# Performance work log

Measured on AMD Instinct MI355X. Metric: run time of the kernel, lower is better.

The kernel has to match this reference:

```python
import jax, jax.numpy as jnp
import numpy as np

NN_SIZE = 10  # k nearest neighbors (includes the point itself)
EPS = 1e-8


def batch_normals(points_nchw, nn_size):
    # points_nchw: (B, 3, N)
    x = jnp.transpose(points_nchw, (0, 2, 1))  # (B, N, 3)
    sq = jnp.sum(x * x, axis=-1)  # (B, N)
    # pairwise squared distances (B, N, N)
    d2 = sq[:, :, None] + sq[:, None, :] - 2.0 * jnp.einsum('bnd,bmd->bnm', x, x)
    _, idx = jax.lax.top_k(-d2, nn_size)  # (B, N, k) nearest-neighbor indices
    # irregular gather of neighborhoods: (B, N, k, 3)
    neigh = jax.vmap(lambda p, i: p[i])(x, idx)
    centered = neigh - jnp.mean(neigh, axis=2, keepdims=True)
    # local 3x3 covariance per point
    cov = jnp.einsum('bnki,bnkj->bnij', centered, centered) / nn_size
    _, vecs = jnp.linalg.eigh(cov)  # eigenvalues ascending
    normals = vecs[..., 0]  # eigenvector of smallest eigenvalue, (B, N, 3), unit norm
    return jnp.transpose(normals, (0, 2, 1))  # (B, 3, N)


def setup_inputs() -> dict:
    key = jax.random.key(0)
    k1, k2 = jax.random.split(key)
    pred = jax.random.normal(k1, (8, 3, 4096), dtype=jnp.float32)
    gt = jax.random.normal(k2, (8, 3, 4096), dtype=jnp.float32)
    return {"pred": pred, "gt": gt}


def reference(pred, gt):
    pn = batch_normals(pred, NN_SIZE)  # (B, 3, N)
    gn = batch_normals(gt, NN_SIZE)    # (B, 3, N)
    # cosine similarity along the channel (coordinate) dim
    dot = jnp.sum(pn * gn, axis=1)
    denom = jnp.sqrt(jnp.sum(pn * pn, axis=1)) * jnp.sqrt(jnp.sum(gn * gn, axis=1))
    cos = dot / jnp.maximum(denom, EPS)
    return jnp.mean(1.0 - jnp.abs(cos))
```

## Files before the change

### kernel.cpp

```cpp
#include <hip/hip_runtime.h>
#include <float.h>
#include <math.h>

#define BATCH 8
#define NPTS 4096
#define KNN 10
#define BN (BATCH * NPTS)

__device__ inline float med3f(float x, float a, float b) {
    return __builtin_amdgcn_fmed3f(x, a, b);
}

__device__ inline void smallest_eigvec(float a00, float a01, float a02,
                                       float a11, float a12, float a22,
                                       float& vx, float& vy, float& vz) {
    float p1 = a01 * a01 + a02 * a02 + a12 * a12;
    float q = (a00 + a11 + a22) * (1.0f / 3.0f);
    float b00 = a00 - q, b11 = a11 - q, b22 = a22 - q;
    float p2 = b00 * b00 + b11 * b11 + b22 * b22 + 2.0f * p1;
    float p = sqrtf(p2 * (1.0f / 6.0f));
    if (p < 1e-20f) { vx = 1.0f; vy = 0.0f; vz = 0.0f; return; }
    float ip = 1.0f / p;
    float c00 = b00 * ip, c01 = a01 * ip, c02 = a02 * ip;
    float c11 = b11 * ip, c12 = a12 * ip, c22 = b22 * ip;
    float detB = c00 * (c11 * c22 - c12 * c12)
               - c01 * (c01 * c22 - c12 * c02)
               + c02 * (c01 * c12 - c11 * c02);
    float r = 0.5f * detB;
    r = fminf(1.0f, fmaxf(-1.0f, r));
    float phi = acosf(r) * (1.0f / 3.0f);
    float lmin = q + 2.0f * p * cosf(phi + 2.0943951023931953f);

    float m00 = a00 - lmin, m11 = a11 - lmin, m22 = a22 - lmin;
    float r0x = m00, r0y = a01, r0z = a02;
    float r1x = a01, r1y = m11, r1z = a12;
    float r2x = a02, r2y = a12, r2z = m22;
    float c0x = r0y * r1z - r0z * r1y, c0y = r0z * r1x - r0x * r1z, c0z = r0x * r1y - r0y * r1x;
    float c1x = r0y * r2z - r0z * r2y, c1y = r0z * r2x - r0x * r2z, c1z = r0x * r2y - r0y * r2x;
    float c2x = r1y * r2z - r1z * r2y, c2y = r1z * r2x - r1x * r2z, c2z = r1x * r2y - r1y * r2x;
    float n0 = c0x * c0x + c0y * c0y + c0z * c0z;
    float n1 = c1x * c1x + c1y * c1y + c1z * c1z;
    float n2 = c2x * c2x + c2y * c2y + c2z * c2z;
    float bx = c0x, by = c0y, bz = c0z, bn = n0;
    if (n1 > bn) { bx = c1x; by = c1y; bz = c1z; bn = n1; }
    if (n2 > bn) { bx = c2x; by = c2y; bz = c2z; bn = n2; }
    if (bn < 1e-30f) { vx = 1.0f; vy = 0.0f; vz = 0.0f; return; }
    float inv = rsqrtf(bn);
    vx = bx * inv; vy = by * inv; vz = bz * inv;
}

__global__ __launch_bounds__(256, 2) void knn_normals_kernel(
    const float* __restrict__ pred, const float* __restrict__ gt,
    float* __restrict__ normals ) {
    __shared__ float sx[NPTS], sy[NPTS], sz[NPTS];
    __shared__ float keybuf[128 * KNN];

    const int b = blockIdx.y;
    const int cloud = blockIdx.z;
    const float* base = (cloud == 0 ? pred : gt) + b * 3 * NPTS;
    const int tid = threadIdx.x;

    for (int i = tid; i < NPTS; i += 256) {
        sx[i] = base[i];
        sy[i] = base[NPTS + i];
        sz[i] = base[2 * NPTS + i];
    }
    __syncthreads();

    const int lp = tid & 127;
    const int seg = tid >> 7;
    const int pt = blockIdx.x * 128 + lp;
    const float mex = sx[pt], mey = sy[pt], mez = sz[pt];

    float k[KNN];
#pragma unroll
    for (int j = 0; j < KNN; ++j) k[j] = FLT_MAX;

    const int m0 = seg * (NPTS / 2);
#pragma unroll 8
    for (int mm = 0; mm < NPTS / 2; ++mm) {
        const int m = m0 + mm;
        float dx = sx[m] - mex;
        float dy = sy[m] - mey;
        float dz = sz[m] - mez;
        float d = dx * dx + dy * dy + dz * dz;
        d = fmaxf(d, 1e-20f);
        float key = __uint_as_float((__float_as_uint(d) & 0xFFFFF000u) | (unsigned)m);
#pragma unroll
        for (int j = KNN - 1; j >= 1; --j) k[j] = med3f(key, k[j - 1], k[j]);
        k[0] = fminf(key, k[0]);
    }

    if (seg == 1) {
#pragma unroll
        for (int j = 0; j < KNN; ++j) keybuf[lp * KNN + j] = k[j];
    }
    __syncthreads();

    if (seg == 0) {
#pragma unroll
        for (int jj = 0; jj < KNN; ++jj) {
            float key = keybuf[lp * KNN + jj];
#pragma unroll
            for (int j = KNN - 1; j >= 1; --j) k[j] = med3f(key, k[j - 1], k[j]);
            k[0] = fminf(key, k[0]);
        }

        float nx[KNN], ny[KNN], nz[KNN];
        float mx = 0.f, my = 0.f, mz = 0.f;
#pragma unroll
        for (int j = 0; j < KNN; ++j) {
            int idx = (int)(__float_as_uint(k[j]) & 0xFFFu);
            nx[j] = sx[idx]; ny[j] = sy[idx]; nz[j] = sz[idx];
            mx += nx[j]; my += ny[j]; mz += nz[j];
        }
        mx *= (1.0f / KNN); my *= (1.0f / KNN); mz *= (1.0f / KNN);

        float cxx = 0.f, cxy = 0.f, cxz = 0.f, cyy = 0.f, cyz = 0.f, czz = 0.f;
#pragma unroll
        for (int j = 0; j < KNN; ++j) {
            float dx = nx[j] - mx, dy = ny[j] - my, dz = nz[j] - mz;
            cxx += dx * dx; cxy += dx * dy; cxz += dx * dz;
            cyy += dy * dy; cyz += dy * dz; czz += dz * dz;
        }
        cxx *= (1.0f / KNN); cxy *= (1.0f / KNN); cxz *= (1.0f / KNN);
        cyy *= (1.0f / KNN); cyz *= (1.0f / KNN); czz *= (1.0f / KNN);

        float vx, vy, vz;
        smallest_eigvec(cxx, cxy, cxz, cyy, cyz, czz, vx, vy, vz);

        float* outp = normals + cloud * 3 * BN;
        const int oidx = b * NPTS + pt;
        outp[oidx] = vx;
        outp[BN + oidx] = vy;
        outp[2 * BN + oidx] = vz;
    }
}

__global__ void zero_out_kernel(float* __restrict__ out) {
    if (threadIdx.x == 0) out[0] = 0.0f;
}

__global__ __launch_bounds__(256) void loss_kernel(const float* __restrict__ normals,
                                                   float* __restrict__ out) {
    __shared__ float red[256];
    const float* pn = normals;
    const float* gn = normals + 3 * BN;
    float acc = 0.f;
    for (int i = blockIdx.x * 256 + threadIdx.x; i < BN; i += 64 * 256) {
        float px = pn[i], py = pn[BN + i], pz = pn[2 * BN + i];
        float gx = gn[i], gy = gn[BN + i], gz = gn[2 * BN + i];
        float dot = px * gx + py * gy + pz * gz;
        float npn = sqrtf(px * px + py * py + pz * pz);
        float ngn = sqrtf(gx * gx + gy * gy + gz * gz);
        float denom = fmaxf(npn * ngn, 1e-8f);
        acc += 1.0f - fabsf(dot / denom);
    }
    red[threadIdx.x] = acc;
    __syncthreads();
    for (int s = 128; s > 0; s >>= 1) {
        if (threadIdx.x < s) red[threadIdx.x] += red[threadIdx.x + s];
        __syncthreads();
    }
    if (threadIdx.x == 0) atomicAdd(out, red[0] * (1.0f / BN));
}

extern "C" void kernel_launch(void* const* d_in, const int* in_sizes, int n_in,
                              void* d_out, int out_size, void* d_ws, size_t ws_size,
                              hipStream_t stream) {
    const float* pred = (const float*)d_in[0];
    const float* gt = (const float*)d_in[1];
    float* out = (float*)d_out;
    float* normals = (float*)d_ws;

    dim3 grid(NPTS / 128, BATCH, 2);
    knn_normals_kernel<<<grid, 256, 0, stream>>>(pred, gt, normals);
    zero_out_kernel<<<1, 64, 0, stream>>>(out);
    loss_kernel<<<64, 256, 0, stream>>>(normals, out);
}
```

Measured before the change: 203.6 us.

## Restructure KNN kernel: 64 queries per block, 4 segments, float4 staged halves

Each block now handles 64 query points split across 4 candidate segments instead of 128 queries across 2. Candidates are staged into shared memory in two halves as float4 (x,y,z,|p|^2), so each distance is three FMAs against precomputed -2*query terms. This halves shared memory and raises the occupancy hint to 4 blocks per SM. The costs are twice the blocks reloading candidates, an extra barrier pass, a longer merge of 30 partial keys, and neighbour coordinates gathered from global memory. The expanded-form distance can also go slightly negative or lose precision, which is clamped to 1e-30.

```diff
diff --git a/kernel.cpp b/kernel.cpp
--- a/kernel.cpp
+++ b/kernel.cpp
@@ -6,6 +6,10 @@
 #define NPTS 4096
 #define KNN 10
 #define BN (BATCH * NPTS)
+#define QPB 64
+#define SEGS 4
+#define HALF (NPTS / 2)
+#define SEGC (HALF / SEGS)
 
 __device__ inline float med3f(float x, float a, float b) {
     return __builtin_amdgcn_fmed3f(x, a, b);
@@ -41,69 +45,78 @@
     float n0 = c0x * c0x + c0y * c0y + c0z * c0z;
     float n1 = c1x * c1x + c1y * c1y + c1z * c1z;
     float n2 = c2x * c2x + c2y * c2y + c2z * c2z;
-    float bx = c0x, by = c0y, bz = c0z, bn = n0;
-    if (n1 > bn) { bx = c1x; by = c1y; bz = c1z; bn = n1; }
-    if (n2 > bn) { bx = c2x; by = c2y; bz = c2z; bn = n2; }
-    if (bn < 1e-30f) { vx = 1.0f; vy = 0.0f; vz = 0.0f; return; }
-    float inv = rsqrtf(bn);
+    float bx = c0x, by = c0y, bz = c0z, bnm = n0;
+    if (n1 > bnm) { bx = c1x; by = c1y; bz = c1z; bnm = n1; }
+    if (n2 > bnm) { bx = c2x; by = c2y; bz = c2z; bnm = n2; }
+    if (bnm < 1e-30f) { vx = 1.0f; vy = 0.0f; vz = 0.0f; return; }
+    float inv = rsqrtf(bnm);
     vx = bx * inv; vy = by * inv; vz = bz * inv;
 }
 
-__global__ __launch_bounds__(256, 2) void knn_normals_kernel(
+__global__ __launch_bounds__(256, 4) void knn_normals_kernel(
     const float* __restrict__ pred, const float* __restrict__ gt,
     float* __restrict__ normals ) {
-    __shared__ float sx[NPTS], sy[NPTS], sz[NPTS];
-    __shared__ float keybuf[128 * KNN];
+    __shared__ float4 pts[HALF];
+    __shared__ float keybuf[3 * QPB * KNN];
 
     const int b = blockIdx.y;
     const int cloud = blockIdx.z;
-    const float* base = (cloud == 0 ? pred : gt) + b * 3 * NPTS;
+    const float* __restrict__ base = (cloud == 0 ? pred : gt) + b * 3 * NPTS;
     const int tid = threadIdx.x;
+    const int q = tid & (QPB - 1);
+    const int seg = tid >> 6;
+    const int pt = blockIdx.x * QPB + q;
 
-    for (int i = tid; i < NPTS; i += 256) {
-        sx[i] = base[i];
-        sy[i] = base[NPTS + i];
-        sz[i] = base[2 * NPTS + i];
-    }
-    __syncthreads();
-
-    const int lp = tid & 127;
-    const int seg = tid >> 7;
-    const int pt = blockIdx.x * 128 + lp;
-    const float mex = sx[pt], mey = sy[pt], mez = sz[pt];
+    const float mex = base[pt];
+    const float mey = base[NPTS + pt];
+    const float mez = base[2 * NPTS + pt];
+    const float nmx = -2.0f * mex, nmy = -2.0f * mey, nmz = -2.0f * mez;
+    const float smw = mex * mex + mey * mey + mez * mez;
 
     float k[KNN];
 #pragma unroll
     for (int j = 0; j < KNN; ++j) k[j] = FLT_MAX;
 
-    const int m0 = seg * (NPTS / 2);
+    for (int pass = 0; pass < 2; ++pass) {
+        const int pb = pass * HALF;
+        for (int i = tid; i < HALF; i += 256) {
+            float x = base[pb + i];
+            float y = base[NPTS + pb + i];
+            float z = base[2 * NPTS + pb + i];
+            pts[i] = make_float4(x, y, z, x * x + y * y + z * z);
+        }
+        __syncthreads();
+
+        const int s0 = seg * SEGC;
+        const unsigned gbase = (unsigned)(pb + s0);
 #pragma unroll 8
-    for (int mm = 0; mm < NPTS / 2; ++mm) {
-        const int m = m0 + mm;
-        float dx = sx[m] - mex;
-        float dy = sy[m] - mey;
-        float dz = sz[m] - mez;
-        float d = dx * dx + dy * dy + dz * dz;
-        d = fmaxf(d, 1e-20f);
-        float key = __uint_as_float((__float_as_uint(d) & 0xFFFFF000u) | (unsigned)m);
+        for (int c = 0; c < SEGC; ++c) {
+            float4 p = pts[s0 + c];
+            float d = fmaf(p.z, nmz, fmaf(p.y, nmy, fmaf(p.x, nmx, p.w + smw)));
+            d = fmaxf(d, 1e-30f);
+            float key = __uint_as_float((__float_as_uint(d) & 0xFFFFF000u) | (gbase + c));
 #pragma unroll
-        for (int j = KNN - 1; j >= 1; --j) k[j] = med3f(key, k[j - 1], k[j]);
-        k[0] = fminf(key, k[0]);
+            for (int j = KNN - 1; j >= 1; --j) k[j] = med3f(key, k[j - 1], k[j]);
+            k[0] = fminf(key, k[0]);
+        }
+        __syncthreads();
     }
 
-    if (seg == 1) {
+    if (seg != 0) {
 #pragma unroll
-        for (int j = 0; j < KNN; ++j) keybuf[lp * KNN + j] = k[j];
+        for (int j = 0; j < KNN; ++j) keybuf[((seg - 1) * QPB + q) * KNN + j] = k[j];
     }
     __syncthreads();
 
     if (seg == 0) {
+        for (int s = 0; s < 3; ++s) {
 #pragma unroll
-        for (int jj = 0; jj < KNN; ++jj) {
-            float key = keybuf[lp * KNN + jj];
+            for (int jj = 0; jj < KNN; ++jj) {
+                float key = keybuf[(s * QPB + q) * KNN + jj];
 #pragma unroll
-            for (int j = KNN - 1; j >= 1; --j) k[j] = med3f(key, k[j - 1], k[j]);
-            k[0] = fminf(key, k[0]);
+                for (int j = KNN - 1; j >= 1; --j) k[j] = med3f(key, k[j - 1], k[j]);
+                k[0] = fminf(key, k[0]);
+            }
         }
 
         float nx[KNN], ny[KNN], nz[KNN];
@@ -111,7 +124,7 @@
 #pragma unroll
         for (int j = 0; j < KNN; ++j) {
             int idx = (int)(__float_as_uint(k[j]) & 0xFFFu);
-            nx[j] = sx[idx]; ny[j] = sy[idx]; nz[j] = sz[idx];
+            nx[j] = base[idx]; ny[j] = base[NPTS + idx]; nz[j] = base[2 * NPTS + idx];
             mx += nx[j]; my += ny[j]; mz += nz[j];
         }
         mx *= (1.0f / KNN); my *= (1.0f / KNN); mz *= (1.0f / KNN);
@@ -173,7 +186,7 @@
     float* out = (float*)d_out;
     float* normals = (float*)d_ws;
 
-    dim3 grid(NPTS / 128, BATCH, 2);
+    dim3 grid(NPTS / QPB, BATCH, 2);
     knn_normals_kernel<<<grid, 256, 0, stream>>>(pred, gt, normals);
     zero_out_kernel<<<1, 64, 0, stream>>>(out);
     loss_kernel<<<64, 256, 0, stream>>>(normals, out);
```

Result: faster. 180.2 us (-11.5%).
